# Optimization experiments

Measured on AMD Instinct MI355X. Metric: run time of the kernel, lower is better.

The kernel has to match this reference:

```python
import jax, jax.numpy as jnp
import numpy as np

EPS = 1e-12  # F.normalize eps


def setup_inputs() -> dict:
    key = jax.random.key(0)
    k1, k2 = jax.random.split(key)
    bs, d = 8192, 128
    data = jax.random.normal(k1, (bs, d), dtype=jnp.float32)
    label = jax.random.randint(k2, (bs, 1), 0, 2, dtype=jnp.int64)
    scale = jnp.asarray(np.log(1.0 / 0.07), dtype=jnp.float32)  # learned temperature param
    return {"data": data, "scale": scale, "label": label}


def reference(data, scale, label):
    bs = data.shape[0]
    # L2-normalize rows (F.normalize semantics with eps clamp)
    norm = jnp.maximum(jnp.linalg.norm(data, axis=-1, keepdims=True), EPS)
    x = data / norm
    logits = (x @ x.T) * jnp.exp(scale)  # [bs, bs]
    # Vectorized equivalent of the python double loop: binary same-class matrix
    sim = (label == label.T).astype(logits.dtype)  # [bs, bs]
    q = jax.nn.softmax(sim / jnp.sum(sim, axis=-1, keepdims=True), axis=-1)
    p = jax.nn.log_softmax(logits, axis=-1)
    log_q = jnp.log(q)  # q > 0 always (softmax output)
    # F.kl_div(p, q, 'batchmean') = sum(q * (log q - p)) / bs
    loss1 = jnp.sum(q * (log_q - p)) / bs
    # F.kl_div(q.log(), p.exp(), 'batchmean') = sum(exp(p) * (p - log q)) / bs
    loss2 = jnp.sum(jnp.exp(p) * (p - log_q)) / bs
    return (loss1 + loss2) * 0.5
```

## Files before the change

### kernel.cpp

```cpp
#include <hip/hip_runtime.h>
#include <stdint.h>

#define BS 8192
#define DD 128
#define SPLIT 16

typedef __attribute__((ext_vector_type(8))) short short8;
typedef __attribute__((ext_vector_type(4))) float float4v;

#if __has_builtin(__builtin_amdgcn_exp2f)
#define EXP2(x) __builtin_amdgcn_exp2f(x)
#else
#define EXP2(x) exp2f(x)
#endif

__device__ __forceinline__ float bf2f(short s) {
  union { unsigned u; float f; } c;
  c.u = ((unsigned)(unsigned short)s) << 16;
  return c.f;
}
__device__ __forceinline__ short f2bf(float f) {
  union { float f; unsigned u; } c; c.f = f;
  unsigned u = c.u + 0x7FFFu + ((c.u >> 16) & 1u);
  return (short)(u >> 16);
}

__global__ __launch_bounds__(256) void k_norm(const float* __restrict__ data,
                                              const int* __restrict__ label,
                                              unsigned int* __restrict__ xnb32,
                                              float* __restrict__ xnf,
                                              float* __restrict__ gh,
                                              int* __restrict__ cnt,
                                              float* __restrict__ Zr,
                                              float* __restrict__ Ur,
                                              float* __restrict__ Vr,
                                              float* __restrict__ mf,
                                              float* __restrict__ out) {
  __shared__ float sh[256];
  __shared__ int shc[2];
  int tid = threadIdx.x, wave = tid >> 6, lane = tid & 63;
  if (tid < 2) shc[tid] = 0;
  sh[tid] = 0.f;
  if (tid < 32) {
    int row = blockIdx.x * 32 + tid;
    Zr[row] = 0.f; Ur[row] = 0.f; Vr[row] = 0.f;
    mf[row] = (label[row] == 0) ? 1.f : 0.f;
  }
  if (blockIdx.x == 0 && tid == 0) out[0] = 0.f;
  __syncthreads();
  float a00 = 0.f, a01 = 0.f, a10 = 0.f, a11 = 0.f;
  int c0 = 0, c1 = 0;
  int rbase = blockIdx.x * 32 + wave * 8;
  for (int r = 0; r < 8; ++r) {
    int row = rbase + r;
    float2 v = *(const float2*)&data[row * DD + lane * 2];
    float ss = v.x * v.x + v.y * v.y;
    for (int off = 32; off; off >>= 1) ss += __shfl_xor(ss, off);
    float rn = 1.f / fmaxf(sqrtf(ss), 1e-12f);
    float x0 = v.x * rn, x1 = v.y * rn;
    *(float2*)&xnf[row * DD + lane * 2] = make_float2(x0, x1);
    unsigned int pk = (unsigned int)(unsigned short)f2bf(x0) |
                      ((unsigned int)(unsigned short)f2bf(x1) << 16);
    xnb32[row * 64 + lane] = pk;
    int lab = label[row];
    if (lab == 0) { a00 += x0; a01 += x1; c0++; }
    else          { a10 += x0; a11 += x1; c1++; }
  }
  atomicAdd(&sh[2 * lane], a00);
  atomicAdd(&sh[2 * lane + 1], a01);
  atomicAdd(&sh[128 + 2 * lane], a10);
  atomicAdd(&sh[128 + 2 * lane + 1], a11);
  if (lane == 0) { atomicAdd(&shc[0], c0); atomicAdd(&shc[1], c1); }
  __syncthreads();
  atomicAdd(&gh[tid], sh[tid]);
  if (tid < 2) atomicAdd(&cnt[tid], shc[tid]);
}

__device__ __forceinline__ void stage_tile(const char* srcbase, int j0,
                                           char* dstbase, int tid) {
  int rowloc = tid >> 4;
  int swz = (tid & 15) ^ rowloc;
  char* dst = dstbase + tid * 16;
#pragma unroll
  for (int p = 0; p < 4; ++p) {
    const char* src = srcbase + (size_t)(j0 + p * 16 + rowloc) * 256 + swz * 16;
    __builtin_amdgcn_global_load_lds(
        (const __attribute__((address_space(1))) void*)(uintptr_t)src,
        (__attribute__((address_space(3))) void*)(uintptr_t)(dst + p * 4096), 16, 0, 0);
  }
}

__device__ __forceinline__ void consume_tile(const short* __restrict__ tile, int j0,
                                             const float* __restrict__ mf,
                                             const short8 afrag[2][4], int quad, int col,
                                             float Z[2][4], float U[2][4], float V0[2][4]) {
#pragma unroll
  for (int jo = 0; jo < 4; ++jo) {
    int jc = j0 + jo * 16 + col;
    float m0 = mf[jc];
    float4v c0 = {0.f, 0.f, 0.f, 0.f}, c1 = {0.f, 0.f, 0.f, 0.f};
    const short* bp = tile + (jo * 16 + col) * DD;
#pragma unroll
    for (int t = 0; t < 4; ++t) {
      short8 b = *(const short8*)(bp + ((t * 4 + quad) ^ col) * 8);
      c0 = __builtin_amdgcn_mfma_f32_16x16x32_bf16(afrag[0][t], b, c0, 0, 0, 0);
      c1 = __builtin_amdgcn_mfma_f32_16x16x32_bf16(afrag[1][t], b, c1, 0, 0, 0);
    }
#pragma unroll
    for (int r = 0; r < 4; ++r) {
      float l0 = c0[r], e0 = EXP2(l0);
      Z[0][r] += e0; U[0][r] += e0 * l0; V0[0][r] += m0 * e0;
      float l1 = c1[r], e1 = EXP2(l1);
      Z[1][r] += e1; U[1][r] += e1 * l1; V0[1][r] += m0 * e1;
    }
  }
}

__global__ __launch_bounds__(256) void k_main(const unsigned short* __restrict__ xnb,
                                              const int* __restrict__ label,
                                              const float* __restrict__ mf,
                                              const float* __restrict__ scale,
                                              float* __restrict__ Zr,
                                              float* __restrict__ Ur,
                                              float* __restrict__ Vr) {
  __shared__ short tileA[64 * DD];
  __shared__ short tileB[64 * DD];
  int tid = threadIdx.x, wave = tid >> 6, lane = tid & 63;
  int quad = lane >> 4, col = lane & 15;
  int rb = blockIdx.x / SPLIT, sl = blockIdx.x % SPLIT;
  float se2 = __expf(scale[0]) * 1.4426950408889634f;

  short8 afrag[2][4];
  int labI[2][4];
#pragma unroll
  for (int s = 0; s < 2; ++s) {
    int arow = rb * 128 + s * 64 + wave * 16 + col;
    const short* ap = (const short*)xnb + (size_t)arow * DD;
#pragma unroll
    for (int t = 0; t < 4; ++t) {
      short8 a = *(const short8*)(ap + t * 32 + quad * 8);
#pragma unroll
      for (int i = 0; i < 8; ++i) a[i] = f2bf(bf2f(a[i]) * se2);
      afrag[s][t] = a;
    }
#pragma unroll
    for (int r = 0; r < 4; ++r)
      labI[s][r] = label[rb * 128 + s * 64 + wave * 16 + quad * 4 + r];
  }

  float Z[2][4] = {}, U[2][4] = {}, V0[2][4] = {};

  const char* srcbase = (const char*)xnb;
  int jbase = sl * (BS / SPLIT), jend = jbase + (BS / SPLIT);

  stage_tile(srcbase, jbase, (char*)tileA, tid);
  __syncthreads();
  for (int j0 = jbase; j0 < jend; j0 += 128) {
    stage_tile(srcbase, j0 + 64, (char*)tileB, tid);
    consume_tile(tileA, j0, mf, afrag, quad, col, Z, U, V0);
    __syncthreads();
    int jn = (j0 + 128 < jend) ? (j0 + 128) : jbase;
    stage_tile(srcbase, jn, (char*)tileA, tid);
    consume_tile(tileB, j0 + 64, mf, afrag, quad, col, Z, U, V0);
    __syncthreads();
  }

#pragma unroll
  for (int s = 0; s < 2; ++s)
#pragma unroll
    for (int r = 0; r < 4; ++r)
#pragma unroll
      for (int off = 1; off < 16; off <<= 1) {
        Z[s][r] += __shfl_xor(Z[s][r], off);
        U[s][r] += __shfl_xor(U[s][r], off);
        V0[s][r] += __shfl_xor(V0[s][r], off);
      }
  if (col == 0) {
#pragma unroll
    for (int s = 0; s < 2; ++s)
#pragma unroll
      for (int r = 0; r < 4; ++r) {
        int row = rb * 128 + s * 64 + wave * 16 + quad * 4 + r;
        float v = (labI[s][r] == 0) ? V0[s][r] : (Z[s][r] - V0[s][r]);
        atomicAdd(&Zr[row], Z[s][r]);
        atomicAdd(&Ur[row], U[s][r] * 0.6931471805599453f);
        atomicAdd(&Vr[row], v);
      }
  }
}

__global__ __launch_bounds__(256) void k_final(const float* __restrict__ xnf,
                                               const int* __restrict__ label,
                                               const float* __restrict__ scale,
                                               const float* __restrict__ gh,
                                               const int* __restrict__ cnt,
                                               const float* __restrict__ Zr,
                                               const float* __restrict__ Ur,
                                               const float* __restrict__ Vr,
                                               float* __restrict__ out) {
  __shared__ float bsum[4];
  int tid = threadIdx.x, wave = tid >> 6, lane = tid & 63;
  float se = __expf(scale[0]);
  float h0a = gh[2 * lane], h0b = gh[2 * lane + 1];
  float h1a = gh[128 + 2 * lane], h1b = gh[128 + 2 * lane + 1];
  float ga = h0a + h1a, gb = h0b + h1b;
  float c0 = (float)cnt[0], c1 = (float)cnt[1];
  float local = 0.f;
  int rbase = blockIdx.x * 32 + wave * 8;
  for (int r = 0; r < 8; ++r) {
    int row = rbase + r;
    float2 x = *(const float2*)&xnf[row * DD + lane * 2];
    int lab = label[row];
    float sg = x.x * ga + x.y * gb;
    float sh_ = (lab == 0) ? (x.x * h0a + x.y * h0b) : (x.x * h1a + x.y * h1b);
    for (int off = 32; off; off >>= 1) {
      sg += __shfl_xor(sg, off);
      sh_ += __shfl_xor(sh_, off);
    }
    if (lane == 0) {
      float cc = (lab == 0) ? c0 : c1;
      float a = __expf(1.f / cc);
      float Zq = cc * a + ((float)BS - cc);
      float S = se * sg, T = se * sh_;
      float Z = Zr[row], U = Ur[row], V = Vr[row];
      local += a / Zq - (S + (a - 1.f) * T) / Zq + U / Z - V / (cc * Z);
    }
  }
  if (lane == 0) bsum[wave] = local;
  __syncthreads();
  if (tid == 0) {
    float s = bsum[0] + bsum[1] + bsum[2] + bsum[3];
    atomicAdd(out, s * (0.5f / (float)BS));
  }
}

extern "C" void kernel_launch(void* const* d_in, const int* in_sizes, int n_in,
                              void* d_out, int out_size, void* d_ws, size_t ws_size,
                              hipStream_t stream) {
  const float* data = (const float*)d_in[0];
  const float* scale = (const float*)d_in[1];
  const int* label = (const int*)d_in[2];
  char* ws = (char*)d_ws;
  unsigned short* xnb = (unsigned short*)ws;
  unsigned int* xnb32 = (unsigned int*)ws;
  float* xnf = (float*)(ws + 2097152);
  float* Zr = (float*)(ws + 6291456);
  float* Ur = (float*)(ws + 6324224);
  float* Vr = (float*)(ws + 6356992);
  float* gh = (float*)(ws + 6389760);
  int* cnt = (int*)(ws + 6390784);
  float* mf = (float*)(ws + 6390800);

  hipMemsetAsync(ws + 6389760, 0, 1032, stream);

  k_norm<<<256, 256, 0, stream>>>(data, label, xnb32, xnf, gh, cnt, Zr, Ur, Vr, mf,
                                  (float*)d_out);
  k_main<<<64 * SPLIT, 256, 0, stream>>>(xnb, label, mf, scale, Zr, Ur, Vr);
  k_final<<<256, 256, 0, stream>>>(xnf, label, scale, gh, cnt, Zr, Ur, Vr, (float*)d_out);
}
```

Measured before the change: 121.0 us.

## Store normalized rows in MFMA fragment layout and read B directly from global memory

k_norm now writes bf16 rows in a pre-swizzled fragment-major layout, so k_main loads A and B operands straight from global memory with register double-buffering instead of staging tiles through LDS. Each wave now covers 64 rows (4 A fragments) over a 256-column slice with SPLIT 32, which gives more reuse per B load, and launch bounds request 3 blocks per CU. The fp32 normalized copy is dropped: k_final recomputes the norm from the raw data, and the group-sum atomics are spread over 4 replicas. Relying on L2 rather than LDS for B reuse and holding more fragments in registers may raise register pressure or memory traffic.

```diff
diff --git a/kernel.cpp b/kernel.cpp
--- a/kernel.cpp
+++ b/kernel.cpp
@@ -3,7 +3,9 @@
 
 #define BS 8192
 #define DD 128
-#define SPLIT 16
+#define SPLIT 32
+#define L2E 1.4426950408889634f
+#define LN2 0.6931471805599453f
 
 typedef __attribute__((ext_vector_type(8))) short short8;
 typedef __attribute__((ext_vector_type(4))) float float4v;
@@ -25,148 +27,128 @@
   return (short)(u >> 16);
 }
 
+
 __global__ __launch_bounds__(256) void k_norm(const float* __restrict__ data,
                                               const int* __restrict__ label,
-                                              unsigned int* __restrict__ xnb32,
-                                              float* __restrict__ xnf,
-                                              float* __restrict__ gh,
+                                              char* __restrict__ xnbF,
+                                              float* __restrict__ gh4,
                                               int* __restrict__ cnt,
                                               float* __restrict__ Zr,
                                               float* __restrict__ Ur,
                                               float* __restrict__ Vr,
                                               float* __restrict__ mf,
                                               float* __restrict__ out) {
-  __shared__ float sh[256];
+  __shared__ float shg[256];
   __shared__ int shc[2];
   int tid = threadIdx.x, wave = tid >> 6, lane = tid & 63;
+  int lh = lane & 31, rsel = lane >> 5;
   if (tid < 2) shc[tid] = 0;
-  sh[tid] = 0.f;
-  if (tid < 32) {
-    int row = blockIdx.x * 32 + tid;
+  shg[tid] = 0.f;
+  int rowbase = blockIdx.x * 8;
+  if (tid < 8) {
+    int row = rowbase + tid;
     Zr[row] = 0.f; Ur[row] = 0.f; Vr[row] = 0.f;
     mf[row] = (label[row] == 0) ? 1.f : 0.f;
   }
   if (blockIdx.x == 0 && tid == 0) out[0] = 0.f;
   __syncthreads();
-  float a00 = 0.f, a01 = 0.f, a10 = 0.f, a11 = 0.f;
-  int c0 = 0, c1 = 0;
-  int rbase = blockIdx.x * 32 + wave * 8;
-  for (int r = 0; r < 8; ++r) {
-    int row = rbase + r;
-    float2 v = *(const float2*)&data[row * DD + lane * 2];
-    float ss = v.x * v.x + v.y * v.y;
-    for (int off = 32; off; off >>= 1) ss += __shfl_xor(ss, off);
-    float rn = 1.f / fmaxf(sqrtf(ss), 1e-12f);
-    float x0 = v.x * rn, x1 = v.y * rn;
-    *(float2*)&xnf[row * DD + lane * 2] = make_float2(x0, x1);
-    unsigned int pk = (unsigned int)(unsigned short)f2bf(x0) |
-                      ((unsigned int)(unsigned short)f2bf(x1) << 16);
-    xnb32[row * 64 + lane] = pk;
-    int lab = label[row];
-    if (lab == 0) { a00 += x0; a01 += x1; c0++; }
-    else          { a10 += x0; a11 += x1; c1++; }
-  }
-  atomicAdd(&sh[2 * lane], a00);
-  atomicAdd(&sh[2 * lane + 1], a01);
-  atomicAdd(&sh[128 + 2 * lane], a10);
-  atomicAdd(&sh[128 + 2 * lane + 1], a11);
-  if (lane == 0) { atomicAdd(&shc[0], c0); atomicAdd(&shc[1], c1); }
-  __syncthreads();
-  atomicAdd(&gh[tid], sh[tid]);
+
+  int row = rowbase + wave * 2 + rsel;
+  float4 v = *(const float4*)&data[row * DD + lh * 4];
+  float ss = v.x * v.x + v.y * v.y + v.z * v.z + v.w * v.w;
+#pragma unroll
+  for (int off = 16; off; off >>= 1) ss += __shfl_xor(ss, off);
+  float rn = 1.f / fmaxf(sqrtf(ss), 1e-12f);
+  float x0 = v.x * rn, x1 = v.y * rn, x2 = v.z * rn, x3 = v.w * rn;
+
+  unsigned pk0 = (unsigned)(unsigned short)f2bf(x0) |
+                 ((unsigned)(unsigned short)f2bf(x1) << 16);
+  unsigned pk1 = (unsigned)(unsigned short)f2bf(x2) |
+                 ((unsigned)(unsigned short)f2bf(x3) << 16);
+  int kc = lh >> 1;
+  size_t chunk = (size_t)(row >> 4) * 256 + (size_t)(kc >> 2) * 64 +
+                 (size_t)(kc & 3) * 16 + (row & 15);
+  *(uint2*)(xnbF + chunk * 16 + (lh & 1) * 8) = make_uint2(pk0, pk1);
+
+  int lab = label[row];
+  int base = lab * 128 + lh * 4;
+  atomicAdd(&shg[base + 0], x0);
+  atomicAdd(&shg[base + 1], x1);
+  atomicAdd(&shg[base + 2], x2);
+  atomicAdd(&shg[base + 3], x3);
+  if (lh == 0) atomicAdd(&shc[lab], 1);
+  __syncthreads();
+  atomicAdd(&gh4[(blockIdx.x & 3) * 256 + tid], shg[tid]);
   if (tid < 2) atomicAdd(&cnt[tid], shc[tid]);
 }
 
-__device__ __forceinline__ void stage_tile(const char* srcbase, int j0,
-                                           char* dstbase, int tid) {
-  int rowloc = tid >> 4;
-  int swz = (tid & 15) ^ rowloc;
-  char* dst = dstbase + tid * 16;
-#pragma unroll
-  for (int p = 0; p < 4; ++p) {
-    const char* src = srcbase + (size_t)(j0 + p * 16 + rowloc) * 256 + swz * 16;
-    __builtin_amdgcn_global_load_lds(
-        (const __attribute__((address_space(1))) void*)(uintptr_t)src,
-        (__attribute__((address_space(3))) void*)(uintptr_t)(dst + p * 4096), 16, 0, 0);
-  }
-}
-
-__device__ __forceinline__ void consume_tile(const short* __restrict__ tile, int j0,
-                                             const float* __restrict__ mf,
-                                             const short8 afrag[2][4], int quad, int col,
-                                             float Z[2][4], float U[2][4], float V0[2][4]) {
-#pragma unroll
-  for (int jo = 0; jo < 4; ++jo) {
-    int jc = j0 + jo * 16 + col;
-    float m0 = mf[jc];
-    float4v c0 = {0.f, 0.f, 0.f, 0.f}, c1 = {0.f, 0.f, 0.f, 0.f};
-    const short* bp = tile + (jo * 16 + col) * DD;
-#pragma unroll
-    for (int t = 0; t < 4; ++t) {
-      short8 b = *(const short8*)(bp + ((t * 4 + quad) ^ col) * 8);
-      c0 = __builtin_amdgcn_mfma_f32_16x16x32_bf16(afrag[0][t], b, c0, 0, 0, 0);
-      c1 = __builtin_amdgcn_mfma_f32_16x16x32_bf16(afrag[1][t], b, c1, 0, 0, 0);
+__device__ __forceinline__ void consume(const short8 af[4][4], short8 b0, short8 b1,
+                                        short8 b2, short8 b3, float m0,
+                                        float Z[4][4], float U[4][4], float V0[4][4]) {
+#pragma unroll
+  for (int s = 0; s < 4; ++s) {
+    float4v c = {0.f, 0.f, 0.f, 0.f};
+    c = __builtin_amdgcn_mfma_f32_16x16x32_bf16(af[s][0], b0, c, 0, 0, 0);
+    c = __builtin_amdgcn_mfma_f32_16x16x32_bf16(af[s][1], b1, c, 0, 0, 0);
+    c = __builtin_amdgcn_mfma_f32_16x16x32_bf16(af[s][2], b2, c, 0, 0, 0);
+    c = __builtin_amdgcn_mfma_f32_16x16x32_bf16(af[s][3], b3, c, 0, 0, 0);
+#pragma unroll
+    for (int r = 0; r < 4; ++r) {
+      float l = c[r], e = EXP2(l);
+      Z[s][r] += e;
+      U[s][r] = fmaf(e, l, U[s][r]);
+      V0[s][r] = fmaf(m0, e, V0[s][r]);
     }
-#pragma unroll
-    for (int r = 0; r < 4; ++r) {
-      float l0 = c0[r], e0 = EXP2(l0);
-      Z[0][r] += e0; U[0][r] += e0 * l0; V0[0][r] += m0 * e0;
-      float l1 = c1[r], e1 = EXP2(l1);
-      Z[1][r] += e1; U[1][r] += e1 * l1; V0[1][r] += m0 * e1;
-    }
-  }
-}
-
-__global__ __launch_bounds__(256) void k_main(const unsigned short* __restrict__ xnb,
-                                              const int* __restrict__ label,
-                                              const float* __restrict__ mf,
-                                              const float* __restrict__ scale,
-                                              float* __restrict__ Zr,
-                                              float* __restrict__ Ur,
-                                              float* __restrict__ Vr) {
-  __shared__ short tileA[64 * DD];
-  __shared__ short tileB[64 * DD];
+  }
+}
+
+__global__ __launch_bounds__(256, 3) void k_main(const short* __restrict__ xnbF,
+                                                 const int* __restrict__ label,
+                                                 const float* __restrict__ mf,
+                                                 const float* __restrict__ scale,
+                                                 float* __restrict__ Zr,
+                                                 float* __restrict__ Ur,
+                                                 float* __restrict__ Vr) {
   int tid = threadIdx.x, wave = tid >> 6, lane = tid & 63;
   int quad = lane >> 4, col = lane & 15;
-  int rb = blockIdx.x / SPLIT, sl = blockIdx.x % SPLIT;
-  float se2 = __expf(scale[0]) * 1.4426950408889634f;
-
-  short8 afrag[2][4];
-  int labI[2][4];
-#pragma unroll
-  for (int s = 0; s < 2; ++s) {
-    int arow = rb * 128 + s * 64 + wave * 16 + col;
-    const short* ap = (const short*)xnb + (size_t)arow * DD;
+  int rbI = blockIdx.x >> 5;
+  int sl = blockIdx.x & 31;
+  float se2 = __expf(scale[0]) * L2E;
+
+  const short8* F = (const short8*)xnbF;
+
+  int gA = rbI * 16 + wave * 4;
+  short8 af[4][4];
+#pragma unroll
+  for (int s = 0; s < 4; ++s)
 #pragma unroll
     for (int t = 0; t < 4; ++t) {
-      short8 a = *(const short8*)(ap + t * 32 + quad * 8);
+      short8 a = F[(size_t)(gA + s) * 256 + t * 64 + lane];
 #pragma unroll
       for (int i = 0; i < 8; ++i) a[i] = f2bf(bf2f(a[i]) * se2);
-      afrag[s][t] = a;
+      af[s][t] = a;
     }
-#pragma unroll
-    for (int r = 0; r < 4; ++r)
-      labI[s][r] = label[rb * 128 + s * 64 + wave * 16 + quad * 4 + r];
-  }
-
-  float Z[2][4] = {}, U[2][4] = {}, V0[2][4] = {};
-
-  const char* srcbase = (const char*)xnb;
-  int jbase = sl * (BS / SPLIT), jend = jbase + (BS / SPLIT);
-
-  stage_tile(srcbase, jbase, (char*)tileA, tid);
-  __syncthreads();
-  for (int j0 = jbase; j0 < jend; j0 += 128) {
-    stage_tile(srcbase, j0 + 64, (char*)tileB, tid);
-    consume_tile(tileA, j0, mf, afrag, quad, col, Z, U, V0);
-    __syncthreads();
-    int jn = (j0 + 128 < jend) ? (j0 + 128) : jbase;
-    stage_tile(srcbase, jn, (char*)tileA, tid);
-    consume_tile(tileB, j0 + 64, mf, afrag, quad, col, Z, U, V0);
-    __syncthreads();
-  }
-
-#pragma unroll
-  for (int s = 0; s < 2; ++s)
+
+  float Z[4][4] = {}, U[4][4] = {}, V0[4][4] = {};
+
+  int gB0 = sl * 16;
+  const short8* FB = F + (size_t)gB0 * 256 + lane;
+
+  short8 a0 = FB[0], a1 = FB[64], a2 = FB[128], a3 = FB[192];
+  float am = mf[gB0 * 16 + col];
+  for (int gg = 0; gg < 16; ++gg) {
+    short8 b0 = a0, b1 = a1, b2 = a2, b3 = a3;
+    float bm = am;
+    if (gg < 15) {
+      const short8* np = FB + (size_t)(gg + 1) * 256;
+      a0 = np[0]; a1 = np[64]; a2 = np[128]; a3 = np[192];
+      am = mf[(gB0 + gg + 1) * 16 + col];
+    }
+    consume(af, b0, b1, b2, b3, bm, Z, U, V0);
+  }
+
+#pragma unroll
+  for (int s = 0; s < 4; ++s)
 #pragma unroll
     for (int r = 0; r < 4; ++r)
 #pragma unroll
@@ -176,60 +158,73 @@
         V0[s][r] += __shfl_xor(V0[s][r], off);
       }
   if (col == 0) {
-#pragma unroll
-    for (int s = 0; s < 2; ++s)
+    int rowb = rbI * 256 + wave * 64;
+#pragma unroll
+    for (int s = 0; s < 4; ++s)
 #pragma unroll
       for (int r = 0; r < 4; ++r) {
-        int row = rb * 128 + s * 64 + wave * 16 + quad * 4 + r;
-        float v = (labI[s][r] == 0) ? V0[s][r] : (Z[s][r] - V0[s][r]);
+        int row = rowb + s * 16 + quad * 4 + r;
+        int lab = label[row];
+        float v = (lab == 0) ? V0[s][r] : (Z[s][r] - V0[s][r]);
         atomicAdd(&Zr[row], Z[s][r]);
-        atomicAdd(&Ur[row], U[s][r] * 0.6931471805599453f);
+        atomicAdd(&Ur[row], U[s][r] * LN2);
         atomicAdd(&Vr[row], v);
       }
   }
 }
 
-__global__ __launch_bounds__(256) void k_final(const float* __restrict__ xnf,
+__global__ __launch_bounds__(256) void k_final(const float* __restrict__ data,
                                                const int* __restrict__ label,
                                                const float* __restrict__ scale,
-                                               const float* __restrict__ gh,
+                                               const float* __restrict__ gh4,
                                                const int* __restrict__ cnt,
                                                const float* __restrict__ Zr,
                                                const float* __restrict__ Ur,
                                                const float* __restrict__ Vr,
                                                float* __restrict__ out) {
-  __shared__ float bsum[4];
+  __shared__ float hsum[256];
+  __shared__ float bsum[8];
   int tid = threadIdx.x, wave = tid >> 6, lane = tid & 63;
+  int lh = lane & 31, rsel = lane >> 5;
+  hsum[tid] = gh4[tid] + gh4[256 + tid] + gh4[512 + tid] + gh4[768 + tid];
+  __syncthreads();
+
   float se = __expf(scale[0]);
-  float h0a = gh[2 * lane], h0b = gh[2 * lane + 1];
-  float h1a = gh[128 + 2 * lane], h1b = gh[128 + 2 * lane + 1];
-  float ga = h0a + h1a, gb = h0b + h1b;
   float c0 = (float)cnt[0], c1 = (float)cnt[1];
-  float local = 0.f;
-  int rbase = blockIdx.x * 32 + wave * 8;
-  for (int r = 0; r < 8; ++r) {
-    int row = rbase + r;
-    float2 x = *(const float2*)&xnf[row * DD + lane * 2];
-    int lab = label[row];
-    float sg = x.x * ga + x.y * gb;
-    float sh_ = (lab == 0) ? (x.x * h0a + x.y * h0b) : (x.x * h1a + x.y * h1b);
-    for (int off = 32; off; off >>= 1) {
-      sg += __shfl_xor(sg, off);
-      sh_ += __shfl_xor(sh_, off);
-    }
-    if (lane == 0) {
-      float cc = (lab == 0) ? c0 : c1;
-      float a = __expf(1.f / cc);
-      float Zq = cc * a + ((float)BS - cc);
-      float S = se * sg, T = se * sh_;
-      float Z = Zr[row], U = Ur[row], V = Vr[row];
-      local += a / Zq - (S + (a - 1.f) * T) / Zq + U / Z - V / (cc * Z);
-    }
-  }
-  if (lane == 0) bsum[wave] = local;
+  int row = blockIdx.x * 8 + wave * 2 + rsel;
+  float4 v = *(const float4*)&data[row * DD + lh * 4];
+  float ss = v.x * v.x + v.y * v.y + v.z * v.z + v.w * v.w;
+#pragma unroll
+  for (int off = 16; off; off >>= 1) ss += __shfl_xor(ss, off);
+  float rn = 1.f / fmaxf(sqrtf(ss), 1e-12f);
+
+  float4 h0 = *(const float4*)&hsum[lh * 4];
+  float4 h1 = *(const float4*)&hsum[128 + lh * 4];
+  int lab = label[row];
+  float sg = v.x * (h0.x + h1.x) + v.y * (h0.y + h1.y) +
+             v.z * (h0.z + h1.z) + v.w * (h0.w + h1.w);
+  float sh_ = (lab == 0)
+                  ? (v.x * h0.x + v.y * h0.y + v.z * h0.z + v.w * h0.w)
+                  : (v.x * h1.x + v.y * h1.y + v.z * h1.z + v.w * h1.w);
+#pragma unroll
+  for (int off = 16; off; off >>= 1) {
+    sg += __shfl_xor(sg, off);
+    sh_ += __shfl_xor(sh_, off);
+  }
+  if (lh == 0) {
+    float cc = (lab == 0) ? c0 : c1;
+    float a = __expf(1.f / cc);
+    float Zq = cc * a + ((float)BS - cc);
+    float S = se * sg * rn, T = se * sh_ * rn;
+    float Zv = Zr[row], Uv = Ur[row], Vv = Vr[row];
+    bsum[wave * 2 + rsel] =
+        a / Zq - (S + (a - 1.f) * T) / Zq + Uv / Zv - Vv / (cc * Zv);
+  }
   __syncthreads();
   if (tid == 0) {
-    float s = bsum[0] + bsum[1] + bsum[2] + bsum[3];
+    float s = 0.f;
+#pragma unroll
+    for (int i = 0; i < 8; ++i) s += bsum[i];
     atomicAdd(out, s * (0.5f / (float)BS));
   }
 }
@@ -241,20 +236,19 @@
   const float* scale = (const float*)d_in[1];
   const int* label = (const int*)d_in[2];
   char* ws = (char*)d_ws;
-  unsigned short* xnb = (unsigned short*)ws;
-  unsigned int* xnb32 = (unsigned int*)ws;
-  float* xnf = (float*)(ws + 2097152);
-  float* Zr = (float*)(ws + 6291456);
-  float* Ur = (float*)(ws + 6324224);
-  float* Vr = (float*)(ws + 6356992);
-  float* gh = (float*)(ws + 6389760);
-  int* cnt = (int*)(ws + 6390784);
-  float* mf = (float*)(ws + 6390800);
-
-  hipMemsetAsync(ws + 6389760, 0, 1032, stream);
-
-  k_norm<<<256, 256, 0, stream>>>(data, label, xnb32, xnf, gh, cnt, Zr, Ur, Vr, mf,
-                                  (float*)d_out);
-  k_main<<<64 * SPLIT, 256, 0, stream>>>(xnb, label, mf, scale, Zr, Ur, Vr);
-  k_final<<<256, 256, 0, stream>>>(xnf, label, scale, gh, cnt, Zr, Ur, Vr, (float*)d_out);
-}
+  char* xnbF = ws;
+  float* Zr = (float*)(ws + 2097152);
+  float* Ur = (float*)(ws + 2129920);
+  float* Vr = (float*)(ws + 2162688);
+  float* gh4 = (float*)(ws + 2195456);
+  int* cnt = (int*)(ws + 2199552);
+  float* mf = (float*)(ws + 2199560);
+
+  hipMemsetAsync(ws + 2195456, 0, 4104, stream);
+
+  k_norm<<<1024, 256, 0, stream>>>(data, label, xnbF, gh4, cnt, Zr, Ur, Vr, mf,
+                                   (float*)d_out);
+  k_main<<<1024, 256, 0, stream>>>((const short*)xnbF, label, mf, scale, Zr, Ur, Vr);
+  k_final<<<1024, 256, 0, stream>>>(data, label, scale, gh4, cnt, Zr, Ur, Vr,
+                                    (float*)d_out);
+}
```

After: 143.3 us. 1.18x slower.
